# Performance work log

Hardware: AMD Instinct MI355X
Metric: run time of the kernel (lower is better)

## Reference

```python
import jax, jax.numpy as jnp
import numpy as np

B, N, C, K = 8, 4096, 128, 9
EPS = 1e-5


def setup_inputs() -> dict:
    key = jax.random.key(0)
    ks = jax.random.split(key, 8)
    x = jax.random.normal(ks[0], (B, N, C), jnp.float32)
    # fc1: Linear(C,C) + BN(C)
    W1 = jax.random.normal(ks[1], (C, C), jnp.float32) * 0.02
    b1 = jnp.zeros((C,), jnp.float32)
    g1 = jnp.ones((C,), jnp.float32)
    be1 = jnp.zeros((C,), jnp.float32)
    # graph conv MLP: Linear(2C,C) + BN(C) + GELU
    Wg = jax.random.normal(ks[2], (2 * C, C), jnp.float32) * 0.02
    bg = jnp.zeros((C,), jnp.float32)
    gg = jnp.ones((C,), jnp.float32)
    beg = jnp.zeros((C,), jnp.float32)
    # fc2: Linear(C,C) + BN(C)
    W2 = jax.random.normal(ks[3], (C, C), jnp.float32) * 0.02
    b2 = jnp.zeros((C,), jnp.float32)
    g2 = jnp.ones((C,), jnp.float32)
    be2 = jnp.zeros((C,), jnp.float32)
    return {"x": x, "W1": W1, "b1": b1, "g1": g1, "be1": be1,
            "Wg": Wg, "bg": bg, "gg": gg, "beg": beg,
            "W2": W2, "b2": b2, "g2": g2, "be2": be2}


def _bn(h, g, b):
    # BatchNorm1d in training mode: batch stats over the (B*N) axis, biased var
    m = jnp.mean(h, axis=0)
    v = jnp.var(h, axis=0)
    return g * (h - m) * jax.lax.rsqrt(v + EPS) + b


def reference(x, W1, b1, g1, be1, Wg, bg, gg, beg, W2, b2, g2, be2):
    Bd, Nd, Cd = x.shape
    residual = x
    # fc1
    h = _bn(x.reshape(Bd * Nd, Cd) @ W1 + b1, g1, be1).reshape(Bd, Nd, Cd)
    # KNN: pairwise squared distances, k smallest
    sq = jnp.sum(h * h, axis=-1, keepdims=True)              # [B,N,1]
    dist = sq - 2.0 * jnp.einsum('bnc,bmc->bnm', h, h) + sq.transpose(0, 2, 1)
    _, idx = jax.lax.top_k(-dist, K)                          # [B,N,K]
    # gather neighbors [B,N,K,C]
    nbrs = jax.vmap(lambda hb, ib: hb[ib])(h, idx)
    # max-relative aggregation
    agg = jnp.max(nbrs - h[:, :, None, :], axis=2)            # [B,N,C]
    cat = jnp.concatenate([h, agg], axis=-1).reshape(Bd * Nd, 2 * Cd)
    hg = jax.nn.gelu(_bn(cat @ Wg + bg, gg, beg), approximate=False)
    # fc2 + residual
    out = _bn(hg @ W2 + b2, g2, be2).reshape(Bd, Nd, Cd) + residual
    return out
```

## Files before the change

### kernel.cpp

```cpp
#include <hip/hip_runtime.h>
#include <hip/hip_bf16.h>
#include <float.h>
#include <math.h>

#define BB 8
#define NN 4096
#define CC 128
#define MROWS (BB * NN)
#define EPSBN 1e-5f

#define QB 64
#define CT 32
#define NTILE (NN / CT)

typedef __attribute__((ext_vector_type(8))) short bf16x8;
typedef __attribute__((ext_vector_type(4))) float f32x4;

#define GLOBAL_AS __attribute__((address_space(1)))
#define LDS_AS __attribute__((address_space(3)))

__device__ __forceinline__ ushort f2bf(float f) {
  uint u = __float_as_uint(f);
  u = u + 0x7fffu + ((u >> 16) & 1u);
  return (ushort)(u >> 16);
}
__device__ __forceinline__ float bf2f(ushort h) {
  return __uint_as_float(((uint)h) << 16);
}

#define GBM 64
#define GBN 128
#define GBK 32

__global__ __launch_bounds__(256)
void gemm_bias_stats_kernel(const float* __restrict__ A, const float* __restrict__ W,
                            const float* __restrict__ bias, float* __restrict__ out,
                            int M, int K, float* __restrict__ sum,
                            float* __restrict__ sumsq) {
  __shared__ float As[GBK][GBM + 4];
  __shared__ float Ws[GBK][GBN + 4];
  __shared__ float redS[GBN], redS2[GBN];
  int tid = threadIdx.x;
  int m0 = blockIdx.x * GBM;
  int ty = tid >> 4, tx = tid & 15;
  if (tid < GBN) { redS[tid] = 0.f; redS2[tid] = 0.f; }

  float acc[4][8];
#pragma unroll
  for (int i = 0; i < 4; ++i)
#pragma unroll
    for (int j = 0; j < 8; ++j) acc[i][j] = 0.f;

  for (int k0 = 0; k0 < K; k0 += GBK) {
    {
      int row = tid >> 2, ch = tid & 3;
      const float* ap = A + (long)(m0 + row) * K + k0 + ch * 8;
      float4 a0 = *(const float4*)ap;
      float4 a1 = *(const float4*)(ap + 4);
      float av2[8] = {a0.x, a0.y, a0.z, a0.w, a1.x, a1.y, a1.z, a1.w};
#pragma unroll
      for (int e = 0; e < 8; ++e) As[ch * 8 + e][row] = av2[e];
    }
#pragma unroll
    for (int c = 0; c < 4; ++c) {
      int lin = tid + 256 * c;
      int row = lin >> 5, c4 = (lin & 31) * 4;
      *(float4*)&Ws[row][c4] = *(const float4*)&W[(long)(k0 + row) * GBN + c4];
    }
    __syncthreads();
#pragma unroll
    for (int kk = 0; kk < GBK; ++kk) {
      float4 a4 = *(const float4*)&As[kk][ty * 4];
      float4 b0 = *(const float4*)&Ws[kk][tx * 8];
      float4 b1 = *(const float4*)&Ws[kk][tx * 8 + 4];
      float av[4] = {a4.x, a4.y, a4.z, a4.w};
      float bv[8] = {b0.x, b0.y, b0.z, b0.w, b1.x, b1.y, b1.z, b1.w};
#pragma unroll
      for (int i = 0; i < 4; ++i)
#pragma unroll
        for (int j = 0; j < 8; ++j)
          acc[i][j] = fmaf(av[i], bv[j], acc[i][j]);
    }
    __syncthreads();
  }
  float bi[8];
  *(float4*)&bi[0] = *(const float4*)&bias[tx * 8];
  *(float4*)&bi[4] = *(const float4*)&bias[tx * 8 + 4];
  float cs[8], css[8];
#pragma unroll
  for (int j = 0; j < 8; ++j) { cs[j] = 0.f; css[j] = 0.f; }
#pragma unroll
  for (int i = 0; i < 4; ++i) {
    long r = (long)(m0 + ty * 4 + i);
    float o[8];
#pragma unroll
    for (int j = 0; j < 8; ++j) {
      o[j] = acc[i][j] + bi[j];
      cs[j] += o[j];
      css[j] += o[j] * o[j];
    }
    float4 o0 = {o[0], o[1], o[2], o[3]};
    float4 o1 = {o[4], o[5], o[6], o[7]};
    *(float4*)&out[r * GBN + tx * 8] = o0;
    *(float4*)&out[r * GBN + tx * 8 + 4] = o1;
  }
#pragma unroll
  for (int j = 0; j < 8; ++j) {
    atomicAdd(&redS[tx * 8 + j], cs[j]);
    atomicAdd(&redS2[tx * 8 + j], css[j]);
  }
  __syncthreads();
  if (tid < GBN) {
    atomicAdd(&sum[tid], redS[tid]);
    atomicAdd(&sumsq[tid], redS2[tid]);
  }
}

__global__ __launch_bounds__(256)
void bn_split_kernel(const float* __restrict__ X, const float* __restrict__ sum,
                     const float* __restrict__ sumsq, const float* __restrict__ g,
                     const float* __restrict__ be, float* __restrict__ cat,
                     ushort* __restrict__ hHi, ushort* __restrict__ hLo,
                     float* __restrict__ sqv) {
  int gid = blockIdx.x * 256 + threadIdx.x;
  int row = gid >> 5;
  int c4 = (gid & 31) * 4;
  const float inv = 1.0f / (float)MROWS;
  float4 x  = *(const float4*)&X[(long)row * CC + c4];
  float4 sm = *(const float4*)&sum[c4];
  float4 sq = *(const float4*)&sumsq[c4];
  float4 gv = *(const float4*)&g[c4];
  float4 bv = *(const float4*)&be[c4];
  float xv[4] = {x.x, x.y, x.z, x.w};
  float smv[4] = {sm.x, sm.y, sm.z, sm.w};
  float sqv2[4] = {sq.x, sq.y, sq.z, sq.w};
  float ga[4] = {gv.x, gv.y, gv.z, gv.w};
  float ba[4] = {bv.x, bv.y, bv.z, bv.w};
  float h[4];
  ushort hi[4], lo[4];
#pragma unroll
  for (int e = 0; e < 4; ++e) {
    float m = smv[e] * inv;
    float v = sqv2[e] * inv - m * m;
    float sc = ga[e] * rsqrtf(v + EPSBN);
    h[e] = (xv[e] - m) * sc + ba[e];
    hi[e] = f2bf(h[e]);
    lo[e] = f2bf(h[e] - bf2f(hi[e]));
  }
  float4 hv = {h[0], h[1], h[2], h[3]};
  *(float4*)&cat[(long)row * 256 + c4] = hv;
  ushort4 h4 = {hi[0], hi[1], hi[2], hi[3]};
  ushort4 l4 = {lo[0], lo[1], lo[2], lo[3]};
  *(ushort4*)&hHi[(long)row * CC + c4] = h4;
  *(ushort4*)&hLo[(long)row * CC + c4] = l4;
  float s = h[0] * h[0] + h[1] * h[1] + h[2] * h[2] + h[3] * h[3];
#pragma unroll
  for (int off = 16; off >= 1; off >>= 1) s += __shfl_xor(s, off, 64);
  if ((threadIdx.x & 31) == 0) sqv[row] = s;
}

__device__ __forceinline__ void insert9(float (&dk)[9], int (&ik)[9], float s, int idx) {
  bool sh[9];
#pragma unroll
  for (int k = 0; k < 9; ++k) sh[k] = s < dk[k];
#pragma unroll
  for (int k = 8; k >= 1; --k) {
    if (sh[k]) {
      bool up = sh[k - 1];
      dk[k] = up ? dk[k - 1] : s;
      ik[k] = up ? ik[k - 1] : idx;
    }
  }
  if (sh[0]) { dk[0] = s; ik[0] = idx; }
}

__device__ __forceinline__ void insert9_lex(float (&dk)[9], int (&ik)[9], float pd, int pi) {
  bool ins = (pd < dk[8]) || (pd == dk[8] && pi < ik[8]);
  if (ins) {
    bool sh[9];
#pragma unroll
    for (int t = 0; t < 9; ++t)
      sh[t] = (pd < dk[t]) || (pd == dk[t] && pi < ik[t]);
#pragma unroll
    for (int t = 8; t >= 1; --t) {
      if (sh[t]) {
        bool up = sh[t - 1];
        dk[t] = up ? dk[t - 1] : pd;
        ik[t] = up ? ik[t - 1] : pi;
      }
    }
    if (sh[0]) { dk[0] = pd; ik[0] = pi; }
  }
}

#define SCST 68

__global__ __attribute__((amdgpu_flat_work_group_size(256, 256), amdgpu_waves_per_eu(4, 4)))
void knn_agg_kernel(const ushort* __restrict__ hHi, const ushort* __restrict__ hLo,
                    const float* __restrict__ sqv, const float* __restrict__ cat,
                    float* __restrict__ catw) {
  __shared__ ushort csBuf[2 * CT * 128];
  __shared__ float  scoreT[CT * SCST];
  ushort* csHi = csBuf;
  ushort* csLo = csBuf + CT * 128;

  int tid = threadIdx.x;
  int wave = tid >> 6, lane = tid & 63;
  int l15 = lane & 15, quad = lane >> 4;
  int wq = wave >> 1, wc = wave & 1;
  int b = blockIdx.x & 7, qt = blockIdx.x >> 3;
  long brow = (long)b * NN;
  long rowbase = brow + (long)qt * QB;

  bf16x8 aHi[2][4], aLo[2][4];
#pragma unroll
  for (int rg = 0; rg < 2; ++rg) {
    long gq = rowbase + wq * 32 + rg * 16 + l15;
    const ushort* ph = hHi + gq * CC + quad * 8;
    const ushort* pl = hLo + gq * CC + quad * 8;
#pragma unroll
    for (int ks = 0; ks < 4; ++ks) {
      aHi[rg][ks] = *(const bf16x8*)(ph + ks * 32);
      aLo[rg][ks] = *(const bf16x8*)(pl + ks * 32);
    }
  }

  int srcOff[2];
#pragma unroll
  for (int it = 0; it < 2; ++it) {
    int s = (wave * 2 + it) * 64 + lane;
    int r = s >> 4, dp = s & 15;
    int d = dp ^ (r & 7);
    srcOff[it] = r * CC + d * 8;
  }

  float dk[9]; int ik[9];
#pragma unroll
  for (int k = 0; k < 9; ++k) { dk[k] = FLT_MAX; ik[k] = 0x7FFFFFFF; }
  int q = tid & 63, quarter = tid >> 6;

  {
    const ushort* baseH = hHi + brow * CC;
    const ushort* baseL = hLo + brow * CC;
#pragma unroll
    for (int it = 0; it < 2; ++it) {
      int s0 = (wave * 2 + it) * 64;
      __builtin_amdgcn_global_load_lds((const GLOBAL_AS void*)(baseH + srcOff[it]),
                                       (LDS_AS void*)&csHi[s0 * 8], 16, 0, 0);
      __builtin_amdgcn_global_load_lds((const GLOBAL_AS void*)(baseL + srcOff[it]),
                                       (LDS_AS void*)&csLo[s0 * 8], 16, 0, 0);
    }
  }
  __syncthreads();

#pragma unroll 1
  for (int ct = 0; ct < NTILE; ++ct) {
    int crow = wc * 16 + l15;
    float sqc = sqv[brow + (long)ct * CT + crow];
    f32x4 ac[2];
#pragma unroll
    for (int rg = 0; rg < 2; ++rg) { ac[rg].x = 0.f; ac[rg].y = 0.f; ac[rg].z = 0.f; ac[rg].w = 0.f; }
#pragma unroll
    for (int ks = 0; ks < 4; ++ks) {
      int sb = crow * 16 + ((ks * 4 + quad) ^ (crow & 7));
      bf16x8 bHi = *(const bf16x8*)&csHi[sb * 8];
      bf16x8 bLo = *(const bf16x8*)&csLo[sb * 8];
#pragma unroll
      for (int rg = 0; rg < 2; ++rg) {
        ac[rg] = __builtin_amdgcn_mfma_f32_16x16x32_bf16(aHi[rg][ks], bHi, ac[rg], 0, 0, 0);
        ac[rg] = __builtin_amdgcn_mfma_f32_16x16x32_bf16(aHi[rg][ks], bLo, ac[rg], 0, 0, 0);
        ac[rg] = __builtin_amdgcn_mfma_f32_16x16x32_bf16(aLo[rg][ks], bHi, ac[rg], 0, 0, 0);
      }
    }
#pragma unroll
    for (int rg = 0; rg < 2; ++rg) {
      float4 o = {fmaf(-2.f, ac[rg].x, sqc), fmaf(-2.f, ac[rg].y, sqc),
                  fmaf(-2.f, ac[rg].z, sqc), fmaf(-2.f, ac[rg].w, sqc)};
      *(float4*)&scoreT[crow * SCST + wq * 32 + rg * 16 + quad * 4] = o;
    }
    __syncthreads();

    {
      int nt = (ct + 1) & (NTILE - 1);
      const ushort* baseH = hHi + (brow + (long)nt * CT) * CC;
      const ushort* baseL = hLo + (brow + (long)nt * CT) * CC;
#pragma unroll
      for (int it = 0; it < 2; ++it) {
        int s0 = (wave * 2 + it) * 64;
        __builtin_amdgcn_global_load_lds((const GLOBAL_AS void*)(baseH + srcOff[it]),
                                         (LDS_AS void*)&csHi[s0 * 8], 16, 0, 0);
        __builtin_amdgcn_global_load_lds((const GLOBAL_AS void*)(baseL + srcOff[it]),
                                         (LDS_AS void*)&csLo[s0 * 8], 16, 0, 0);
      }
    }

    int gbase = ct * CT + quarter * 8;
    const float* scol = &scoreT[(quarter * 8) * SCST + q];
    float thr = dk[8];
#pragma unroll
    for (int jj = 0; jj < 8; jj += 4) {
      float s0 = scol[(jj + 0) * SCST];
      float s1 = scol[(jj + 1) * SCST];
      float s2 = scol[(jj + 2) * SCST];
      float s3 = scol[(jj + 3) * SCST];
      float mn = fminf(fminf(s0, s1), fminf(s2, s3));
      if (mn < thr) {
        if (s0 < thr) { insert9(dk, ik, s0, gbase + jj + 0); thr = dk[8]; }
        if (s1 < thr) { insert9(dk, ik, s1, gbase + jj + 1); thr = dk[8]; }
        if (s2 < thr) { insert9(dk, ik, s2, gbase + jj + 2); thr = dk[8]; }
        if (s3 < thr) { insert9(dk, ik, s3, gbase + jj + 3); thr = dk[8]; }
      }
    }
    __syncthreads();
  }

  float* mD = (float*)csBuf;
  int*   mI = (int*)csBuf + 1728;
  int*   fI = (int*)csBuf + 3456;
  if (quarter > 0) {
    int base = (quarter - 1) * 576 + q * 9;
#pragma unroll
    for (int k = 0; k < 9; ++k) { mD[base + k] = dk[k]; mI[base + k] = ik[k]; }
  }
  __syncthreads();
  if (quarter == 0) {
#pragma unroll 1
    for (int qq = 0; qq < 3; ++qq) {
      int base = qq * 576 + q * 9;
#pragma unroll 1
      for (int k = 0; k < 9; ++k)
        insert9_lex(dk, ik, mD[base + k], mI[base + k]);
    }
#pragma unroll
    for (int k = 0; k < 9; ++k) fI[q * 9 + k] = ik[k];
  }
  __syncthreads();

  int nb[9];
#pragma unroll
  for (int k = 0; k < 9; ++k) nb[k] = fI[q * 9 + k];
  long qrow = rowbase + q;
  const float4* cat4 = (const float4*)cat;
  float4* catw4 = (float4*)catw;
#pragma unroll 1
  for (int c4 = 0; c4 < 8; ++c4) {
    int cc = quarter * 8 + c4;
    float4 hq = cat4[qrow * 64 + cc];
    float4 mx = {-FLT_MAX, -FLT_MAX, -FLT_MAX, -FLT_MAX};
#pragma unroll
    for (int k = 0; k < 9; ++k) {
      float4 v = cat4[(brow + nb[k]) * 64 + cc];
      mx.x = fmaxf(mx.x, v.x - hq.x);
      mx.y = fmaxf(mx.y, v.y - hq.y);
      mx.z = fmaxf(mx.z, v.z - hq.z);
      mx.w = fmaxf(mx.w, v.w - hq.w);
    }
    catw4[qrow * 64 + 32 + cc] = mx;
  }
}

__global__ __launch_bounds__(256)
void bn_gelu_kernel(const float* __restrict__ X, const float* __restrict__ sum,
                    const float* __restrict__ sumsq, const float* __restrict__ g,
                    const float* __restrict__ be, float* __restrict__ out) {
  int gid = blockIdx.x * 256 + threadIdx.x;
  int row = gid >> 5;
  int c4 = (gid & 31) * 4;
  const float inv = 1.0f / (float)MROWS;
  float4 x  = *(const float4*)&X[(long)row * CC + c4];
  float4 sm = *(const float4*)&sum[c4];
  float4 sq = *(const float4*)&sumsq[c4];
  float4 gv = *(const float4*)&g[c4];
  float4 bv = *(const float4*)&be[c4];
  float xv[4] = {x.x, x.y, x.z, x.w};
  float smv[4] = {sm.x, sm.y, sm.z, sm.w};
  float sqv2[4] = {sq.x, sq.y, sq.z, sq.w};
  float ga[4] = {gv.x, gv.y, gv.z, gv.w};
  float ba[4] = {bv.x, bv.y, bv.z, bv.w};
  float o[4];
#pragma unroll
  for (int e = 0; e < 4; ++e) {
    float m = smv[e] * inv;
    float v = sqv2[e] * inv - m * m;
    float sc = ga[e] * rsqrtf(v + EPSBN);
    float h = (xv[e] - m) * sc + ba[e];
    o[e] = 0.5f * h * (1.0f + erff(h * 0.70710678118654752f));
  }
  float4 ov = {o[0], o[1], o[2], o[3]};
  *(float4*)&out[(long)row * CC + c4] = ov;
}

__global__ __launch_bounds__(256)
void bn_res_kernel(const float* __restrict__ X, const float* __restrict__ sum,
                   const float* __restrict__ sumsq, const float* __restrict__ g,
                   const float* __restrict__ be, const float* __restrict__ xres,
                   float* __restrict__ out) {
  int gid = blockIdx.x * 256 + threadIdx.x;
  int row = gid >> 5;
  int c4 = (gid & 31) * 4;
  const float inv = 1.0f / (float)MROWS;
  float4 x  = *(const float4*)&X[(long)row * CC + c4];
  float4 rr = *(const float4*)&xres[(long)row * CC + c4];
  float4 sm = *(const float4*)&sum[c4];
  float4 sq = *(const float4*)&sumsq[c4];
  float4 gv = *(const float4*)&g[c4];
  float4 bv = *(const float4*)&be[c4];
  float xv[4] = {x.x, x.y, x.z, x.w};
  float rv[4] = {rr.x, rr.y, rr.z, rr.w};
  float smv[4] = {sm.x, sm.y, sm.z, sm.w};
  float sqv2[4] = {sq.x, sq.y, sq.z, sq.w};
  float ga[4] = {gv.x, gv.y, gv.z, gv.w};
  float ba[4] = {bv.x, bv.y, bv.z, bv.w};
  float o[4];
#pragma unroll
  for (int e = 0; e < 4; ++e) {
    float m = smv[e] * inv;
    float v = sqv2[e] * inv - m * m;
    float sc = ga[e] * rsqrtf(v + EPSBN);
    o[e] = (xv[e] - m) * sc + ba[e] + rv[e];
  }
  float4 ov = {o[0], o[1], o[2], o[3]};
  *(float4*)&out[(long)row * CC + c4] = ov;
}

extern "C" void kernel_launch(void* const* d_in, const int* in_sizes, int n_in,
                              void* d_out, int out_size, void* d_ws, size_t ws_size,
                              hipStream_t stream) {
  const float* x   = (const float*)d_in[0];
  const float* W1  = (const float*)d_in[1];
  const float* b1  = (const float*)d_in[2];
  const float* g1  = (const float*)d_in[3];
  const float* be1 = (const float*)d_in[4];
  const float* Wg  = (const float*)d_in[5];
  const float* bg  = (const float*)d_in[6];
  const float* ggp = (const float*)d_in[7];
  const float* beg = (const float*)d_in[8];
  const float* W2  = (const float*)d_in[9];
  const float* b2  = (const float*)d_in[10];
  const float* g2  = (const float*)d_in[11];
  const float* be2 = (const float*)d_in[12];
  float* out = (float*)d_out;

  char* p = (char*)d_ws;
  auto alloc = [&](size_t bytes) {
    char* r = p;
    p += (bytes + 255) & ~(size_t)255;
    return r;
  };
  float*  bufA = (float*)alloc((size_t)MROWS * CC * 4);
  float*  cat  = (float*)alloc((size_t)MROWS * 256 * 4);
  ushort* hHi  = (ushort*)alloc((size_t)MROWS * CC * 2);
  ushort* hLo  = (ushort*)alloc((size_t)MROWS * CC * 2);
  float*  sqv  = (float*)alloc((size_t)MROWS * 4);
  float*  hg   = (float*)alloc((size_t)MROWS * CC * 4);
  float*  stats = (float*)alloc(6 * CC * 4);
  float* sum1 = stats,       *ss1 = stats + 128;
  float* sum2 = stats + 256, *ss2 = stats + 384;
  float* sum3 = stats + 512, *ss3 = stats + 640;

  hipMemsetAsync(stats, 0, 6 * CC * 4, stream);

  gemm_bias_stats_kernel<<<MROWS / GBM, 256, 0, stream>>>(x, W1, b1, bufA, MROWS, CC, sum1, ss1);
  bn_split_kernel<<<MROWS / 8, 256, 0, stream>>>(bufA, sum1, ss1, g1, be1, cat, hHi, hLo, sqv);

  knn_agg_kernel<<<512, 256, 0, stream>>>(hHi, hLo, sqv, cat, cat);

  gemm_bias_stats_kernel<<<MROWS / GBM, 256, 0, stream>>>(cat, Wg, bg, bufA, MROWS, 2 * CC, sum2, ss2);
  bn_gelu_kernel<<<MROWS / 8, 256, 0, stream>>>(bufA, sum2, ss2, ggp, beg, hg);

  gemm_bias_stats_kernel<<<MROWS / GBM, 256, 0, stream>>>(hg, W2, b2, bufA, MROWS, CC, sum3, ss3);
  bn_res_kernel<<<MROWS / 8, 256, 0, stream>>>(bufA, sum3, ss3, g2, be2, x, out);
}
```

Before: 473.7 us.

## Split KNN candidate scan into four slices with a separate merge kernel

The KNN kernel, previously 512 blocks each scanning all 4096 candidates, becomes 2048 blocks that each scan a quarter of the candidate points. Each block writes a partial top-9 list to global memory, and a new merge kernel combines the four partial lists per query before aggregating. This raises the block count to fill more of the device's compute units and shortens the serial tile loop. In exchange it adds a kernel launch, extra global traffic for the partial lists, and reloads the query fragments four times. The waves_per_eu attribute is also dropped in favour of plain launch bounds.

```diff
diff --git a/kernel.cpp b/kernel.cpp
--- a/kernel.cpp
+++ b/kernel.cpp
@@ -11,7 +11,9 @@
 
 #define QB 64
 #define CT 32
-#define NTILE (NN / CT)
+#define SPLIT 4
+#define SLICEN (NN / SPLIT)
+#define NTS (SLICEN / CT)
 
 typedef __attribute__((ext_vector_type(8))) short bf16x8;
 typedef __attribute__((ext_vector_type(4))) float f32x4;
@@ -195,10 +197,10 @@
 
 #define SCST 68
 
-__global__ __attribute__((amdgpu_flat_work_group_size(256, 256), amdgpu_waves_per_eu(4, 4)))
-void knn_agg_kernel(const ushort* __restrict__ hHi, const ushort* __restrict__ hLo,
-                    const float* __restrict__ sqv, const float* __restrict__ cat,
-                    float* __restrict__ catw) {
+__global__ __launch_bounds__(256)
+void knn_part_kernel(const ushort* __restrict__ hHi, const ushort* __restrict__ hLo,
+                     const float* __restrict__ sqv,
+                     float* __restrict__ pD, int* __restrict__ pI) {
   __shared__ ushort csBuf[2 * CT * 128];
   __shared__ float  scoreT[CT * SCST];
   ushort* csHi = csBuf;
@@ -208,9 +210,12 @@
   int wave = tid >> 6, lane = tid & 63;
   int l15 = lane & 15, quad = lane >> 4;
   int wq = wave >> 1, wc = wave & 1;
-  int b = blockIdx.x & 7, qt = blockIdx.x >> 3;
+  int b = blockIdx.x & 7;
+  int t2 = blockIdx.x >> 3;
+  int qt = t2 & 63, slice = t2 >> 6;
   long brow = (long)b * NN;
   long rowbase = brow + (long)qt * QB;
+  long cbase = brow + (long)slice * SLICEN;
 
   bf16x8 aHi[2][4], aLo[2][4];
 #pragma unroll
@@ -240,8 +245,8 @@
   int q = tid & 63, quarter = tid >> 6;
 
   {
-    const ushort* baseH = hHi + brow * CC;
-    const ushort* baseL = hLo + brow * CC;
+    const ushort* baseH = hHi + cbase * CC;
+    const ushort* baseL = hLo + cbase * CC;
 #pragma unroll
     for (int it = 0; it < 2; ++it) {
       int s0 = (wave * 2 + it) * 64;
@@ -254,9 +259,9 @@
   __syncthreads();
 
 #pragma unroll 1
-  for (int ct = 0; ct < NTILE; ++ct) {
+  for (int ct = 0; ct < NTS; ++ct) {
     int crow = wc * 16 + l15;
-    float sqc = sqv[brow + (long)ct * CT + crow];
+    float sqc = sqv[cbase + (long)ct * CT + crow];
     f32x4 ac[2];
 #pragma unroll
     for (int rg = 0; rg < 2; ++rg) { ac[rg].x = 0.f; ac[rg].y = 0.f; ac[rg].z = 0.f; ac[rg].w = 0.f; }
@@ -281,9 +286,9 @@
     __syncthreads();
 
     {
-      int nt = (ct + 1) & (NTILE - 1);
-      const ushort* baseH = hHi + (brow + (long)nt * CT) * CC;
-      const ushort* baseL = hLo + (brow + (long)nt * CT) * CC;
+      int nt = (ct + 1) & (NTS - 1);
+      const ushort* baseH = hHi + (cbase + (long)nt * CT) * CC;
+      const ushort* baseL = hLo + (cbase + (long)nt * CT) * CC;
 #pragma unroll
       for (int it = 0; it < 2; ++it) {
         int s0 = (wave * 2 + it) * 64;
@@ -294,7 +299,7 @@
       }
     }
 
-    int gbase = ct * CT + quarter * 8;
+    int gbase = slice * SLICEN + ct * CT + quarter * 8;
     const float* scol = &scoreT[(quarter * 8) * SCST + q];
     float thr = dk[8];
 #pragma unroll
@@ -316,7 +321,45 @@
 
   float* mD = (float*)csBuf;
   int*   mI = (int*)csBuf + 1728;
-  int*   fI = (int*)csBuf + 3456;
+  if (quarter > 0) {
+    int base = (quarter - 1) * 576 + q * 9;
+#pragma unroll
+    for (int k = 0; k < 9; ++k) { mD[base + k] = dk[k]; mI[base + k] = ik[k]; }
+  }
+  __syncthreads();
+  if (quarter == 0) {
+#pragma unroll 1
+    for (int qq = 0; qq < 3; ++qq) {
+      int base = qq * 576 + q * 9;
+#pragma unroll 1
+      for (int k = 0; k < 9; ++k)
+        insert9_lex(dk, ik, mD[base + k], mI[base + k]);
+    }
+    long pbase = ((long)blockIdx.x) * 576 + q * 9;
+#pragma unroll
+    for (int k = 0; k < 9; ++k) { pD[pbase + k] = dk[k]; pI[pbase + k] = ik[k]; }
+  }
+}
+
+__global__ __launch_bounds__(256)
+void knn_merge_agg_kernel(const float* __restrict__ pD, const int* __restrict__ pI,
+                          const float* __restrict__ cat, float* __restrict__ catw) {
+  __shared__ float mD[3 * 576];
+  __shared__ int   mI[3 * 576];
+  __shared__ int   fI[576];
+
+  int tid = threadIdx.x;
+  int b = blockIdx.x & 7, qt = blockIdx.x >> 3;
+  long brow = (long)b * NN;
+  long rowbase = brow + (long)qt * QB;
+  int q = tid & 63, quarter = tid >> 6;
+
+  float dk[9]; int ik[9];
+  {
+    long pbase = ((long)(b + 8 * (qt + 64 * quarter))) * 576 + q * 9;
+#pragma unroll
+    for (int k = 0; k < 9; ++k) { dk[k] = pD[pbase + k]; ik[k] = pI[pbase + k]; }
+  }
   if (quarter > 0) {
     int base = (quarter - 1) * 576 + q * 9;
 #pragma unroll
@@ -453,6 +496,8 @@
   ushort* hLo  = (ushort*)alloc((size_t)MROWS * CC * 2);
   float*  sqv  = (float*)alloc((size_t)MROWS * 4);
   float*  hg   = (float*)alloc((size_t)MROWS * CC * 4);
+  float*  pD   = (float*)alloc((size_t)2048 * 576 * 4);
+  int*    pI   = (int*)alloc((size_t)2048 * 576 * 4);
   float*  stats = (float*)alloc(6 * CC * 4);
   float* sum1 = stats,       *ss1 = stats + 128;
   float* sum2 = stats + 256, *ss2 = stats + 384;
@@ -463,7 +508,8 @@
   gemm_bias_stats_kernel<<<MROWS / GBM, 256, 0, stream>>>(x, W1, b1, bufA, MROWS, CC, sum1, ss1);
   bn_split_kernel<<<MROWS / 8, 256, 0, stream>>>(bufA, sum1, ss1, g1, be1, cat, hHi, hLo, sqv);
 
-  knn_agg_kernel<<<512, 256, 0, stream>>>(hHi, hLo, sqv, cat, cat);
+  knn_part_kernel<<<2048, 256, 0, stream>>>(hHi, hLo, sqv, pD, pI);
+  knn_merge_agg_kernel<<<512, 256, 0, stream>>>(pD, pI, cat, cat);
 
   gemm_bias_stats_kernel<<<MROWS / GBM, 256, 0, stream>>>(cat, Wg, bg, bufA, MROWS, 2 * CC, sum2, ss2);
   bn_gelu_kernel<<<MROWS / 8, 256, 0, stream>>>(bufA, sum2, ss2, ggp, beg, hg);
```

Measured after the change: 474.9 us. About the same (+0.2%).
